# Performance work log

Measured on AMD Instinct MI355X. Metric: run time of the kernel, lower is better.

The kernel has to match this reference:

```python
import jax, jax.numpy as jnp
import numpy as np

A0 = 0.529177249
SIGMA = jnp.array([0.5515909, 1.8886297, 1.3225029, 1.2316629, 2.1884933, 1.7750372, 1.3677907, 1.3820058], dtype=jnp.float32)
N_MOL, N_ATOM, N_SPECIES = 512, 64, 4
AEV_LEN, RADIAL_LEN = 384, 32
DIN = AEV_LEN + RADIAL_LEN + 2  # 418
DIMS = (256, 192, 160)
ETA, RC = 4.0, 10.0  # stand-in radial-qaev constants (Bohr)
RS = jnp.linspace(0.8, 9.0, RADIAL_LEN, dtype=jnp.float32)


def _celu(x):
    return jax.nn.celu(x, alpha=0.1)


def _mlp(x, W0, b0, W1, b1, W2, b2, W3, b3):
    h = _celu(x @ W0 + b0)
    h = _celu(h @ W1 + b1)
    h = _celu(h @ W2 + b2)
    return (h @ W3 + b3)[:, 0]


def _dispatch(x, species_flat, W0, b0, W1, b1, W2, b2, W3, b3):
    # per-species expert MLP routing; padded atoms (species==-1) stay 0
    out = jnp.zeros(x.shape[0], x.dtype)
    for s in range(N_SPECIES):
        ys = _mlp(x, W0[s], b0[s], W1[s], b1[s], W2[s], b2[s], W3[s], b3[s])
        out = jnp.where(species_flat == s, ys, out)
    return out


def _radial_qaev(d, charges, pair_nodiag):
    # stand-in for compute_radial_qaev: charge-weighted radial symmetry functions
    fc = jnp.where(d < RC, 0.5 * jnp.cos(np.pi * d / RC) + 0.5, 0.0)
    g = 0.25 * jnp.exp(-ETA * (d[..., None] - RS) ** 2) * (fc * pair_nodiag)[..., None]  # [N,n,n,R]
    return jnp.einsum('nijr,nj->nir', g, charges)


def _esperf(pair_mask, diag_mask, d, charges, sig):
    s = jnp.maximum(sig[:, None, :] ** 2 + sig[:, :, None] ** 2, 1e-8)
    j_ij = jax.scipy.special.erf(d / jnp.sqrt(2.0 * s)) / d
    return (charges[:, :, None] * j_ij * pair_mask * diag_mask[None]).sum(axis=-2)


def _forward(species, coordinates, net_charge, aev, chi_params, ani_params):
    N, n = species.shape
    diff = coordinates[:, None, :, :] - coordinates[:, :, None, :]
    d = jnp.sqrt((diff * diff).sum(-1) + 1e-16) / A0  # Bohr, [N,n,n]
    sig = SIGMA[species]  # species==-1 wraps to last entry, matching torch
    inv_jii = np.sqrt(np.pi).astype(np.float32) * sig  # 1 / (1/sqrt(pi)/sig)
    pm = (species != -1).astype(d.dtype)
    pair_mask = pm[:, None, :] * pm[:, :, None]
    diag_mask = 1.0 - jnp.eye(n, dtype=d.dtype)
    pair_nodiag = pair_mask * diag_mask
    species_flat = species.reshape(-1)
    aevf = aev.reshape(N * n, -1)
    q = jnp.zeros((N, n), d.dtype)
    esp = jnp.zeros((N, n), d.dtype)
    qraev = _radial_qaev(d, q, pair_nodiag)
    for _ in range(2):  # charge equilibration loop
        feats = jnp.concatenate([aevf, qraev.reshape(N * n, -1), q.reshape(-1, 1), esp.reshape(-1, 1)], axis=1)
        chi = _dispatch(feats, species_flat, *chi_params).reshape(N, n)
        corr = (net_charge + (chi * inv_jii).sum(1)) / (inv_jii * pm).sum(1)
        q = -inv_jii * (chi - corr[:, None]) * pm
        esp = _esperf(pair_mask, diag_mask, d, q, sig)
        qraev = _radial_qaev(d, q, pair_nodiag)
    feats = jnp.concatenate([aevf, qraev.reshape(N * n, -1), q.reshape(-1, 1), esp.reshape(-1, 1)], axis=1)
    ae = _dispatch(feats, species_flat, *ani_params).reshape(N, n)
    charge_sq = q[:, None, :] * q[:, :, None] * pair_mask
    coulomb = charge_sq * jax.nn.sigmoid((d - 2.2) * 8.5) / d  # elect_screen
    elec = jnp.triu(coulomb, k=1).sum(axis=(1, 2))
    return ae.sum(1) + elec, q


def setup_inputs() -> dict:
    key = jax.random.key(0)
    ks = jax.random.split(key, 5)
    species = jax.random.randint(ks[0], (N_MOL, N_ATOM), -1, N_SPECIES)  # -1 = padding
    coordinates = jax.random.uniform(ks[1], (N_MOL, N_ATOM, 3), jnp.float32) * 10.0
    net_charge = jnp.zeros((N_MOL,), jnp.float32)
    aev = jax.random.normal(ks[2], (N_MOL, N_ATOM, AEV_LEN), jnp.float32)
    inp = {'species': species, 'coordinates': coordinates, 'net_charge': net_charge, 'aev': aev}
    dims = (DIN,) + DIMS + (1,)
    for name, k in (('chi', ks[3]), ('ani', ks[4])):
        lks = jax.random.split(k, 4)
        for i in range(4):
            inp[f'{name}_W{i}'] = jax.random.normal(lks[i], (N_SPECIES, dims[i], dims[i + 1]), jnp.float32) / float(np.sqrt(dims[i]))
            inp[f'{name}_b{i}'] = jnp.zeros((N_SPECIES, dims[i + 1]), jnp.float32)
    return inp


def reference(species, coordinates, net_charge, aev,
              chi_W0, chi_b0, chi_W1, chi_b1, chi_W2, chi_b2, chi_W3, chi_b3,
              ani_W0, ani_b0, ani_W1, ani_b1, ani_W2, ani_b2, ani_W3, ani_b3):
    chi_params = (chi_W0, chi_b0, chi_W1, chi_b1, chi_W2, chi_b2, chi_W3, chi_b3)
    ani_params = (ani_W0, ani_b0, ani_W1, ani_b1, ani_W2, ani_b2, ani_W3, ani_b3)
    energy, q = _forward(species, coordinates, net_charge, aev, chi_params, ani_params)
    return (species, energy, q)
```

## Files before the change

### kernel.cpp

```cpp
#include <hip/hip_runtime.h>
#include <math.h>

#define NMOL 512
#define NATOM 64
#define NFLAT (NMOL*NATOM)
#define AEVL 384
#define FK 448
#define D0 256
#define D1 192
#define D2 160
#define MPAD 33024

typedef _Float16 h8 __attribute__((ext_vector_type(8)));
typedef float    f4 __attribute__((ext_vector_type(4)));

__constant__ float c_sigma[8] = {0.5515909f,1.8886297f,1.3225029f,1.2316629f,
                                 2.1884933f,1.7750372f,1.3677907f,1.3820058f};

__device__ __forceinline__ float wsum(float v){
  #pragma unroll
  for (int o=1;o<64;o<<=1) v += __shfl_xor(v,o);
  return v;
}

__device__ __forceinline__ void gll16(const _Float16* g, _Float16* l){
  __builtin_amdgcn_global_load_lds(
    (const __attribute__((address_space(1))) void*)g,
    (__attribute__((address_space(3))) void*)l, 16, 0, 0);
}

__global__ void cvt_aev_kernel(const float* __restrict__ aev, _Float16* __restrict__ feat){
  int atom = blockIdx.x*4 + (threadIdx.x>>6);
  int c = threadIdx.x & 63;
  if (c >= 56) return;
  int k8 = c*8;
  h8 o;
  if (k8 < AEVL){
    const f4* s = reinterpret_cast<const f4*>(aev + (size_t)atom*AEVL + k8);
    f4 a = s[0], b = s[1];
    o[0]=(_Float16)a[0]; o[1]=(_Float16)a[1]; o[2]=(_Float16)a[2]; o[3]=(_Float16)a[3];
    o[4]=(_Float16)b[0]; o[5]=(_Float16)b[1]; o[6]=(_Float16)b[2]; o[7]=(_Float16)b[3];
  } else {
    #pragma unroll
    for (int i=0;i<8;i++) o[i] = (_Float16)0.f;
  }
  *reinterpret_cast<h8*>(feat + (size_t)atom*FK + k8) = o;
}

__global__ void wtrans_kernel(const float* __restrict__ Wc, const float* __restrict__ Wa,
                              _Float16* __restrict__ WtC, _Float16* __restrict__ WtA,
                              int K, int N, int KT){
  int u = blockIdx.x*256 + threadIdx.x;
  if (u >= KT*4*N) return;
  int col = u % N;
  int pk  = u / N;
  int part = pk & 3, kt = pk >> 2;
  int s = blockIdx.y;
  const float* W = (blockIdx.z == 0) ? Wc : Wa;
  _Float16* Wt   = (blockIdx.z == 0) ? WtC : WtA;
  h8 o;
  #pragma unroll
  for (int e=0;e<8;e++){
    int gk = kt*32 + part*8 + e;
    float v = (gk < K) ? W[((size_t)s*K + gk)*N + col] : 0.f;
    o[e] = (_Float16)v;
  }
  *reinterpret_cast<h8*>(Wt + ((size_t)s*KT*4 + pk)*N*8 + (size_t)col*8) = o;
}

__global__ void prep_kernel(const int* __restrict__ species,
                            const float* __restrict__ coord,
                            float* __restrict__ dbuf, float* __restrict__ sig,
                            float* __restrict__ invj, float* __restrict__ pmf,
                            int* __restrict__ blkhist){
  int m = blockIdx.x, t = threadIdx.x;
  __shared__ float c[192];
  if (t < 192) c[t] = coord[m*192 + t];
  __syncthreads();
  #pragma unroll
  for (int k=0;k<16;k++){
    int p = t + 256*k;
    int i = p >> 6, j = p & 63;
    float dx=c[i*3]-c[j*3], dy=c[i*3+1]-c[j*3+1], dz=c[i*3+2]-c[j*3+2];
    dbuf[m*4096 + p] = sqrtf(dx*dx+dy*dy+dz*dz + 1e-16f) / 0.529177249f;
  }
  if (t < 64){
    int g = m*64+t;
    int s = species[g];
    float sg = c_sigma[s < 0 ? 7 : s];
    sig[g]  = sg;
    invj[g] = 1.7724539f * sg;
    pmf[g]  = (s>=0) ? 1.f : 0.f;
    #pragma unroll
    for (int sp=0;sp<4;sp++){
      unsigned long long mask = __ballot(s==sp);
      if (t==0) blkhist[m*4+sp] = __popcll(mask);
    }
  }
}

__global__ void plan_kernel(const int* __restrict__ blkhist, int* __restrict__ meta,
                            int* __restrict__ blkoff){
  __shared__ int h[NMOL*4];
  __shared__ int tot[4], base[4];
  int t = threadIdx.x;
  for (int j=t; j<NMOL*4; j+=256) h[j] = blkhist[j];
  __syncthreads();
  if (t < 4){
    int sum = 0;
    for (int m=0;m<NMOL;m++) sum += h[m*4+t];
    tot[t] = sum;
  }
  __syncthreads();
  if (t == 0){
    int b=0, tb=0;
    meta[4]=0; meta[9]=0;
    for (int s=0;s<4;s++){
      meta[s] = tot[s];
      base[s] = b;
      int tiles = (tot[s]+63)>>6;
      b  += tiles<<6;  tb += tiles;
      meta[5+s]  = b;  meta[10+s] = tb;
    }
  }
  __syncthreads();
  if (t < 4){
    int run = base[t];
    for (int m=0;m<NMOL;m++){ int v = h[m*4+t]; h[m*4+t] = run; run += v; }
  }
  __syncthreads();
  for (int j=t; j<NMOL*4; j+=256) blkoff[j] = h[j];
}

__global__ void scatter_kernel(const int* __restrict__ species,
                               const int* __restrict__ blkoff,
                               int* __restrict__ idxarr){
  int m = blockIdx.x, a = threadIdx.x, g = m*64+a;
  int s = species[g];
  unsigned long long below = (1ull<<a) - 1ull;
  #pragma unroll
  for (int sp=0;sp<4;sp++){
    unsigned long long mask = __ballot(s==sp);
    if (s==sp){
      int rank = __popcll(mask & below);
      idxarr[blkoff[m*4+sp] + rank] = g;
    }
  }
}

template<int GATHER, int NCB, int KTW, int FUSEL3>
__launch_bounds__(256)
__global__ void gemm_gll(const _Float16* __restrict__ Ah,
                         const _Float16* __restrict__ feat,
                         const int* __restrict__ idxarr,
                         const int* __restrict__ meta,
                         const _Float16* __restrict__ Wt,
                         const float* __restrict__ Ball,
                         _Float16* __restrict__ C,
                         const float* __restrict__ W3a,
                         const float* __restrict__ b3a,
                         float* __restrict__ outv,
                         int N, int ktrun, int act){
  constexpr int COLS = NCB*16;
  constexpr int NB16 = COLS/16;
  int t = blockIdx.x;
  if (t >= meta[13]) return;
  int s = 0;
  while (s < 3 && t >= meta[10+s]) s++;
  int trow = t - meta[9+s];
  int row0 = meta[4+s] + (trow<<6);
  int mrem = meta[s] - (trow<<6); if (mrem > 64) mrem = 64;
  int c0 = blockIdx.y * COLS;

  __shared__ __align__(16) _Float16 Ab[2][2048];
  __shared__ __align__(16) _Float16 Bb[2][COLS*32];

  int tid = threadIdx.x;
  int w = tid>>6, l = tid&63, lr16 = l&15, lg = l>>4;

  int arow = row0 + l;
  int amax = row0 + mrem - 1;
  if (arow > amax) arow = amax;
  const _Float16* asrc;
  if (GATHER) asrc = feat + (size_t)idxarr[arow]*FK;
  else        asrc = Ah + (size_t)arow*(KTW*32);

  const _Float16* Wbase = Wt + (size_t)s*KTW*4*N*8 + (size_t)c0*8;

  auto STAGE = [&](int buf, int kt){
    gll16(asrc + kt*32 + w*8, &Ab[buf][w*512]);
    for (int j=w; j<NB16; j+=4){
      int u = j*64 + l;
      int part = u / COLS, col = u - part*COLS;
      gll16(Wbase + ((size_t)(kt*4+part)*N + col)*8, &Bb[buf][j*512]);
    }
  };

  f4 acc[NCB];
  #pragma unroll
  for (int c=0;c<NCB;c++){ acc[c][0]=0.f; acc[c][1]=0.f; acc[c][2]=0.f; acc[c][3]=0.f; }

  STAGE(0, 0);
  __syncthreads();
  int cur = 0;
  for (int kt=0; kt<ktrun; ++kt){
    if (kt+1 < ktrun) STAGE(cur^1, kt+1);
    h8 aF = *reinterpret_cast<const h8*>(&Ab[cur][lg*512 + (w*16+lr16)*8]);
    #pragma unroll
    for (int c=0;c<NCB;c++){
      h8 bF = *reinterpret_cast<const h8*>(&Bb[cur][lg*COLS*8 + (c*16+lr16)*8]);
      acc[c] = __builtin_amdgcn_mfma_f32_16x16x32_f16(aF, bF, acc[c], 0, 0, 0);
    }
    if (kt+1 < ktrun){
      __syncthreads();
      cur ^= 1;
    }
  }

  const float* bias = Ball + s*N;
  if (FUSEL3){
    const float* w3 = W3a + s*COLS;
    float vrow[4] = {0.f,0.f,0.f,0.f};
    #pragma unroll
    for (int c=0;c<NCB;c++){
      int col = c*16 + lr16;
      float bsv = bias[col];
      float wv  = w3[col];
      #pragma unroll
      for (int rr=0;rr<4;rr++){
        float vv = acc[c][rr] + bsv;
        vv = vv > 0.f ? vv : 0.1f*expm1f(vv*10.f);
        vrow[rr] += vv * wv;
      }
    }
    float b3v = b3a[s];
    #pragma unroll
    for (int rr=0;rr<4;rr++){
      float v = vrow[rr];
      #pragma unroll
      for (int o=1;o<16;o<<=1) v += __shfl_xor(v, o);
      int lrow = w*16 + lg*4 + rr;
      if (lr16 == 0 && lrow < mrem)
        outv[idxarr[row0+lrow]] = v + b3v;
    }
  } else {
    #pragma unroll
    for (int c=0;c<NCB;c++){
      int col = c0 + c*16 + lr16;
      float bsv = bias[col];
      #pragma unroll
      for (int rr=0;rr<4;rr++){
        int lrow = w*16 + lg*4 + rr;
        if (lrow >= mrem) continue;
        float vv = acc[c][rr] + bsv;
        if (act) vv = vv > 0.f ? vv : 0.1f*expm1f(vv*10.f);
        C[(size_t)(row0+lrow)*N + col] = (_Float16)vv;
      }
    }
  }
}

__global__ void iter_kernel(const float* __restrict__ chi, const float* __restrict__ invj,
                            const float* __restrict__ pmf, const float* __restrict__ netq,
                            const float* __restrict__ dbuf, const float* __restrict__ sig,
                            float* __restrict__ q, _Float16* __restrict__ feat){
  int m = blockIdx.x, tid = threadIdx.x;
  int i = tid & 63, w = tid >> 6;
  __shared__ float qs[64], pms[64], sg2[64];
  __shared__ float esp8[8][64];
  __shared__ float qr[8][64][8];
  if (tid < 64){
    int g = m*64 + i;
    float pm = pmf[g], ij = invj[g];
    float c = pm > 0.f ? chi[g] : 0.f;
    float num = wsum(c*ij);
    float den = wsum(ij*pm);
    float corr = (netq[m] + num) / den;
    float qa = -ij*(c - corr)*pm;
    q[g] = qa;
    feat[(size_t)g*FK + 416] = (_Float16)qa;
    qs[i] = qa; pms[i] = pm;
    float s0 = sig[g]; sg2[i] = s0*s0;
  }
  __syncthreads();
  const float* dr = dbuf + (size_t)m*4096;
  {
    float si2 = sg2[i];
    float acc = 0.f;
    #pragma unroll
    for (int jj=0;jj<8;jj++){
      int j = w*8 + jj;
      if (j==i) continue;
      float d = dr[j*64 + i];
      float ss = fmaxf(si2 + sg2[j], 1e-8f);
      acc += qs[j]*pms[j]*erff(d/sqrtf(2.f*ss))/d;
    }
    esp8[w][i] = acc;
  }
  {
    const float STEP = 0.264516129f;
    const float C2 = 0.7558781f;
    const float C1 = 0.5713518f;
    int jh = w>>2, bg = w&3;
    float rbase = 0.8f + (bg*8)*STEP;
    float pmi = pms[i];
    float acc[8] = {0.f,0.f,0.f,0.f,0.f,0.f,0.f,0.f};
    for (int jj=0;jj<32;jj++){
      int j = jh*32 + jj;
      if (j==i) continue;
      float d = dr[j*64+i];
      if (d < 10.f){
        float wq = 0.25f*(0.5f*__cosf(0.31415927f*d)+0.5f)*qs[j]*pms[j]*pmi;
        if (wq != 0.f){
          float t0 = d - rbase;
          float fv = __expf(-4.f*t0*t0);
          float gv = __expf(2.116129f*t0)*C2;
          #pragma unroll
          for (int r=0;r<8;r++){ acc[r] += wq*fv; fv *= gv; gv *= C1; }
        }
      }
    }
    #pragma unroll
    for (int r=0;r<8;r++) qr[w][i][r] = acc[r];
  }
  __syncthreads();
  if (tid < 64){
    int g = m*64+i;
    float e = 0.f;
    #pragma unroll
    for (int k=0;k<8;k++) e += esp8[k][i];
    feat[(size_t)g*FK + 417] = (_Float16)(e * pms[i]);
  }
  if (tid < 256){
    int ii = tid & 63, bg = tid >> 6;
    h8 o;
    #pragma unroll
    for (int r=0;r<8;r++) o[r] = (_Float16)(qr[bg][ii][r] + qr[bg+4][ii][r]);
    *reinterpret_cast<h8*>(feat + (size_t)(m*64+ii)*FK + 384 + bg*8) = o;
  }
}

__global__ void final_kernel(const float* __restrict__ dbuf, const float* __restrict__ q,
                             const float* __restrict__ pmf, const float* __restrict__ ae,
                             const int* __restrict__ species, float* __restrict__ out){
  int m = blockIdx.x, a = threadIdx.x, g = m*64+a;
  __shared__ float qs[64], pms[64];
  qs[a]=q[g]; pms[a]=pmf[g];
  __syncthreads();
  float acc=0.f;
  const float* dr = dbuf + (size_t)m*4096;
  for (int b=0;b<64;b++){
    if (b==a) continue;
    float d = dr[b*64+a];
    float sgm = 1.f/(1.f+__expf(-(d-2.2f)*8.5f));
    acc += qs[b]*pms[b]*sgm/d;
  }
  float e = 0.5f*qs[a]*pms[a]*acc;
  float aea = pms[a]>0.f ? ae[g] : 0.f;
  float tot = wsum(e + aea);
  if (a == 0) out[NFLAT + m] = tot;
  out[g] = (float)species[g];
  out[NFLAT + NMOL + g] = qs[a];
}

extern "C" void kernel_launch(void* const* d_in, const int* in_sizes, int n_in,
                              void* d_out, int out_size, void* d_ws, size_t ws_size,
                              hipStream_t stream){
  const int*   species = (const int*)d_in[0];
  const float* coord   = (const float*)d_in[1];
  const float* netq    = (const float*)d_in[2];
  const float* aev     = (const float*)d_in[3];
  const float* cW[4] = {(const float*)d_in[4],(const float*)d_in[6],(const float*)d_in[8],(const float*)d_in[10]};
  const float* cB[4] = {(const float*)d_in[5],(const float*)d_in[7],(const float*)d_in[9],(const float*)d_in[11]};
  const float* aW[4] = {(const float*)d_in[12],(const float*)d_in[14],(const float*)d_in[16],(const float*)d_in[18]};
  const float* aB[4] = {(const float*)d_in[13],(const float*)d_in[15],(const float*)d_in[17],(const float*)d_in[19]};

  float* f = (float*)d_ws;
  size_t o = 0;
  float* dbuf  = f + o; o += (size_t)NMOL*4096;
  float* sig   = f + o; o += NFLAT;
  float* invj  = f + o; o += NFLAT;
  float* pmf   = f + o; o += NFLAT;
  float* q     = f + o; o += NFLAT;
  float* chi   = f + o; o += NFLAT;
  _Float16* feat = (_Float16*)(f + o); o += (size_t)NFLAT*FK/2;
  _Float16* h0h  = (_Float16*)(f + o); o += (size_t)MPAD*D0/2;
  _Float16* h1h  = (_Float16*)(f + o); o += (size_t)MPAD*D1/2;
  const int KT_[3] = {14, 8, 6};
  const int N_[3]  = {D0, D1, D2};
  _Float16* wt[6];
  for (int i=0;i<6;i++){
    wt[i] = (_Float16*)(f + o);
    o += (size_t)4*KT_[i%3]*N_[i%3]*32/2;
  }
  int* meta    = (int*)(f + o); o += 64;
  int* idxarr  = (int*)(f + o); o += MPAD;
  int* blkhist = (int*)(f + o); o += NMOL*4;
  int* blkoff  = (int*)(f + o); o += NMOL*4;

  cvt_aev_kernel<<<dim3(NFLAT/4), 256, 0, stream>>>(aev, feat);
  for (int li=0; li<3; ++li){
    int K = (li==0) ? 418 : (li==1 ? D0 : D1);
    int N = N_[li], KT = KT_[li];
    wtrans_kernel<<<dim3((KT*4*N+255)/256, 4, 2), 256, 0, stream>>>(
        cW[li], aW[li], wt[li], wt[3+li], K, N, KT);
  }
  prep_kernel<<<dim3(NMOL), 256, 0, stream>>>(species, coord, dbuf, sig, invj, pmf, blkhist);
  plan_kernel<<<dim3(1), 256, 0, stream>>>(blkhist, meta, blkoff);
  scatter_kernel<<<dim3(NMOL), 64, 0, stream>>>(species, blkoff, idxarr);

  for (int pass=0; pass<3; ++pass){
    int wb = (pass<2) ? 0 : 3;
    const float* const* Bp = (pass<2) ? cB : aB;
    const float* W3 = (pass<2) ? cW[3] : aW[3];
    const float* b3 = (pass<2) ? cB[3] : aB[3];
    int kt0 = (pass==0) ? 12 : 14;
    gemm_gll<1,8,14,0><<<dim3(516,2), 256, 0, stream>>>(nullptr, feat, idxarr, meta,
                                                        wt[wb+0], Bp[0], h0h,
                                                        nullptr, nullptr, nullptr, D0, kt0, 1);
    gemm_gll<0,6,8,0><<<dim3(516,2), 256, 0, stream>>>(h0h, nullptr, idxarr, meta,
                                                       wt[wb+1], Bp[1], h1h,
                                                       nullptr, nullptr, nullptr, D1, 8, 1);
    gemm_gll<0,10,6,1><<<dim3(516,1), 256, 0, stream>>>(h1h, nullptr, idxarr, meta,
                                                        wt[wb+2], Bp[2], nullptr,
                                                        W3, b3, chi, D2, 6, 1);
    if (pass < 2)
      iter_kernel<<<dim3(NMOL), 512, 0, stream>>>(chi, invj, pmf, netq, dbuf, sig, q, feat);
  }
  final_kernel<<<dim3(NMOL), 64, 0, stream>>>(dbuf, q, pmf, chi, species, (float*)d_out);
}
```

Baseline: 273.3 us.

## Use full-width column tiles in GEMMs and merge prep launches

```diff
diff --git a/kernel.cpp b/kernel.cpp
--- a/kernel.cpp
+++ b/kernel.cpp
@@ -29,35 +29,22 @@
     (__attribute__((address_space(3))) void*)l, 16, 0, 0);
 }
 
-__global__ void cvt_aev_kernel(const float* __restrict__ aev, _Float16* __restrict__ feat){
-  int atom = blockIdx.x*4 + (threadIdx.x>>6);
-  int c = threadIdx.x & 63;
-  if (c >= 56) return;
-  int k8 = c*8;
-  h8 o;
-  if (k8 < AEVL){
-    const f4* s = reinterpret_cast<const f4*>(aev + (size_t)atom*AEVL + k8);
-    f4 a = s[0], b = s[1];
-    o[0]=(_Float16)a[0]; o[1]=(_Float16)a[1]; o[2]=(_Float16)a[2]; o[3]=(_Float16)a[3];
-    o[4]=(_Float16)b[0]; o[5]=(_Float16)b[1]; o[6]=(_Float16)b[2]; o[7]=(_Float16)b[3];
-  } else {
-    #pragma unroll
-    for (int i=0;i<8;i++) o[i] = (_Float16)0.f;
-  }
-  *reinterpret_cast<h8*>(feat + (size_t)atom*FK + k8) = o;
-}
-
-__global__ void wtrans_kernel(const float* __restrict__ Wc, const float* __restrict__ Wa,
-                              _Float16* __restrict__ WtC, _Float16* __restrict__ WtA,
-                              int K, int N, int KT){
+__global__ void wtrans_all(const float* __restrict__ W0c, const float* __restrict__ W1c,
+                           const float* __restrict__ W2c, const float* __restrict__ W0a,
+                           const float* __restrict__ W1a, const float* __restrict__ W2a,
+                           _Float16* __restrict__ T0c, _Float16* __restrict__ T1c,
+                           _Float16* __restrict__ T2c, _Float16* __restrict__ T0a,
+                           _Float16* __restrict__ T1a, _Float16* __restrict__ T2a){
   int u = blockIdx.x*256 + threadIdx.x;
-  if (u >= KT*4*N) return;
+  int s = blockIdx.y;
+  int ani = blockIdx.z;
+  const float* W; _Float16* T; int K, N, KT;
+  if (u < 14336){            W = ani?W0a:W0c; T = ani?T0a:T0c; K=418; N=256; KT=14; }
+  else if (u < 20480){ u -= 14336; W = ani?W1a:W1c; T = ani?T1a:T1c; K=256; N=192; KT=8; }
+  else               { u -= 20480; W = ani?W2a:W2c; T = ani?T2a:T2c; K=192; N=160; KT=6; }
   int col = u % N;
   int pk  = u / N;
   int part = pk & 3, kt = pk >> 2;
-  int s = blockIdx.y;
-  const float* W = (blockIdx.z == 0) ? Wc : Wa;
-  _Float16* Wt   = (blockIdx.z == 0) ? WtC : WtA;
   h8 o;
   #pragma unroll
   for (int e=0;e<8;e++){
@@ -65,14 +52,15 @@
     float v = (gk < K) ? W[((size_t)s*K + gk)*N + col] : 0.f;
     o[e] = (_Float16)v;
   }
-  *reinterpret_cast<h8*>(Wt + ((size_t)s*KT*4 + pk)*N*8 + (size_t)col*8) = o;
+  *reinterpret_cast<h8*>(T + ((size_t)s*KT*4 + pk)*N*8 + (size_t)col*8) = o;
 }
 
 __global__ void prep_kernel(const int* __restrict__ species,
                             const float* __restrict__ coord,
+                            const float* __restrict__ aev,
                             float* __restrict__ dbuf, float* __restrict__ sig,
                             float* __restrict__ invj, float* __restrict__ pmf,
-                            int* __restrict__ blkhist){
+                            int* __restrict__ blkhist, _Float16* __restrict__ feat){
   int m = blockIdx.x, t = threadIdx.x;
   __shared__ float c[192];
   if (t < 192) c[t] = coord[m*192 + t];
@@ -96,6 +84,23 @@
       unsigned long long mask = __ballot(s==sp);
       if (t==0) blkhist[m*4+sp] = __popcll(mask);
     }
+  }
+  const float* aevm = aev + (size_t)m*64*AEVL;
+  _Float16* featm = feat + (size_t)m*64*FK;
+  for (int j=t; j<64*56; j+=256){
+    int al = j/56, cc = j - (j/56)*56;
+    int k8 = cc*8;
+    h8 o;
+    if (k8 < AEVL){
+      const f4* sp = reinterpret_cast<const f4*>(aevm + (size_t)al*AEVL + k8);
+      f4 a = sp[0], b = sp[1];
+      o[0]=(_Float16)a[0]; o[1]=(_Float16)a[1]; o[2]=(_Float16)a[2]; o[3]=(_Float16)a[3];
+      o[4]=(_Float16)b[0]; o[5]=(_Float16)b[1]; o[6]=(_Float16)b[2]; o[7]=(_Float16)b[3];
+    } else {
+      #pragma unroll
+      for (int e=0;e<8;e++) o[e] = (_Float16)0.f;
+    }
+    *reinterpret_cast<h8*>(featm + (size_t)al*FK + k8) = o;
   }
 }
 
@@ -160,7 +165,7 @@
                          const float* __restrict__ W3a,
                          const float* __restrict__ b3a,
                          float* __restrict__ outv,
-                         int N, int ktrun, int act){
+                         int ktrun, int act){
   constexpr int COLS = NCB*16;
   constexpr int NB16 = COLS/16;
   int t = blockIdx.x;
@@ -170,7 +175,6 @@
   int trow = t - meta[9+s];
   int row0 = meta[4+s] + (trow<<6);
   int mrem = meta[s] - (trow<<6); if (mrem > 64) mrem = 64;
-  int c0 = blockIdx.y * COLS;
 
   __shared__ __align__(16) _Float16 Ab[2][2048];
   __shared__ __align__(16) _Float16 Bb[2][COLS*32];
@@ -185,14 +189,14 @@
   if (GATHER) asrc = feat + (size_t)idxarr[arow]*FK;
   else        asrc = Ah + (size_t)arow*(KTW*32);
 
-  const _Float16* Wbase = Wt + (size_t)s*KTW*4*N*8 + (size_t)c0*8;
+  const _Float16* Wbase = Wt + (size_t)s*KTW*4*COLS*8;
 
   auto STAGE = [&](int buf, int kt){
     gll16(asrc + kt*32 + w*8, &Ab[buf][w*512]);
     for (int j=w; j<NB16; j+=4){
       int u = j*64 + l;
       int part = u / COLS, col = u - part*COLS;
-      gll16(Wbase + ((size_t)(kt*4+part)*N + col)*8, &Bb[buf][j*512]);
+      gll16(Wbase + ((size_t)(kt*4+part)*COLS + col)*8, &Bb[buf][j*512]);
     }
   };
 
@@ -217,7 +221,7 @@
     }
   }
 
-  const float* bias = Ball + s*N;
+  const float* bias = Ball + s*COLS;
   if (FUSEL3){
     const float* w3 = W3a + s*COLS;
     float vrow[4] = {0.f,0.f,0.f,0.f};
@@ -246,7 +250,7 @@
   } else {
     #pragma unroll
     for (int c=0;c<NCB;c++){
-      int col = c0 + c*16 + lr16;
+      int col = c*16 + lr16;
       float bsv = bias[col];
       #pragma unroll
       for (int rr=0;rr<4;rr++){
@@ -254,7 +258,7 @@
         if (lrow >= mrem) continue;
         float vv = acc[c][rr] + bsv;
         if (act) vv = vv > 0.f ? vv : 0.1f*expm1f(vv*10.f);
-        C[(size_t)(row0+lrow)*N + col] = (_Float16)vv;
+        C[(size_t)(row0+lrow)*COLS + col] = (_Float16)vv;
       }
     }
   }
@@ -398,14 +402,10 @@
   int* blkhist = (int*)(f + o); o += NMOL*4;
   int* blkoff  = (int*)(f + o); o += NMOL*4;
 
-  cvt_aev_kernel<<<dim3(NFLAT/4), 256, 0, stream>>>(aev, feat);
-  for (int li=0; li<3; ++li){
-    int K = (li==0) ? 418 : (li==1 ? D0 : D1);
-    int N = N_[li], KT = KT_[li];
-    wtrans_kernel<<<dim3((KT*4*N+255)/256, 4, 2), 256, 0, stream>>>(
-        cW[li], aW[li], wt[li], wt[3+li], K, N, KT);
-  }
-  prep_kernel<<<dim3(NMOL), 256, 0, stream>>>(species, coord, dbuf, sig, invj, pmf, blkhist);
+  prep_kernel<<<dim3(NMOL), 256, 0, stream>>>(species, coord, aev, dbuf, sig, invj, pmf,
+                                              blkhist, feat);
+  wtrans_all<<<dim3(95, 4, 2), 256, 0, stream>>>(cW[0], cW[1], cW[2], aW[0], aW[1], aW[2],
+                                                 wt[0], wt[1], wt[2], wt[3], wt[4], wt[5]);
   plan_kernel<<<dim3(1), 256, 0, stream>>>(blkhist, meta, blkoff);
   scatter_kernel<<<dim3(NMOL), 64, 0, stream>>>(species, blkoff, idxarr);
 
@@ -415,15 +415,15 @@
     const float* W3 = (pass<2) ? cW[3] : aW[3];
     const float* b3 = (pass<2) ? cB[3] : aB[3];
     int kt0 = (pass==0) ? 12 : 14;
-    gemm_gll<1,8,14,0><<<dim3(516,2), 256, 0, stream>>>(nullptr, feat, idxarr, meta,
-                                                        wt[wb+0], Bp[0], h0h,
-                                                        nullptr, nullptr, nullptr, D0, kt0, 1);
-    gemm_gll<0,6,8,0><<<dim3(516,2), 256, 0, stream>>>(h0h, nullptr, idxarr, meta,
-                                                       wt[wb+1], Bp[1], h1h,
-                                                       nullptr, nullptr, nullptr, D1, 8, 1);
-    gemm_gll<0,10,6,1><<<dim3(516,1), 256, 0, stream>>>(h1h, nullptr, idxarr, meta,
-                                                        wt[wb+2], Bp[2], nullptr,
-                                                        W3, b3, chi, D2, 6, 1);
+    gemm_gll<1,16,14,0><<<dim3(516), 256, 0, stream>>>(nullptr, feat, idxarr, meta,
+                                                       wt[wb+0], Bp[0], h0h,
+                                                       nullptr, nullptr, nullptr, kt0, 1);
+    gemm_gll<0,12,8,0><<<dim3(516), 256, 0, stream>>>(h0h, nullptr, idxarr, meta,
+                                                      wt[wb+1], Bp[1], h1h,
+                                                      nullptr, nullptr, nullptr, 8, 1);
+    gemm_gll<0,10,6,1><<<dim3(516), 256, 0, stream>>>(h1h, nullptr, idxarr, meta,
+                                                      wt[wb+2], Bp[2], nullptr,
+                                                      W3, b3, chi, 6, 1);
     if (pass < 2)
       iter_kernel<<<dim3(NMOL), 512, 0, stream>>>(chi, invj, pmf, netq, dbuf, sig, q, feat);
   }
```

After: 307.8 us. 12.6% more time.
